# Optimization experiments

Measured on AMD Instinct MI355X. Metric: run time of the kernel, lower is better.

The kernel has to match this reference:

```python
import jax, jax.numpy as jnp
import numpy as np

N_NODES = 100000
N_HYPEREDGES = 20000
NNZ = 600000
D = 128


def setup_inputs() -> dict:
    key = jax.random.key(0)
    k = jax.random.split(key, 6)
    s = 1.0 / np.sqrt(D)
    x = jax.random.normal(k[0], (N_NODES, D), jnp.float32)
    node_idx = jax.random.randint(k[1], (NNZ,), 0, N_NODES, dtype=jnp.int64 if jax.config.jax_enable_x64 else jnp.int32)
    edge_idx = jax.random.randint(k[2], (NNZ,), 0, N_HYPEREDGES, dtype=jnp.int64 if jax.config.jax_enable_x64 else jnp.int32)
    conv_W = jax.random.uniform(k[3], (D, D), jnp.float32, -s, s)
    conv_b = jnp.zeros((D,), jnp.float32)
    res_W = jax.random.uniform(k[4], (D, D), jnp.float32, -s, s)
    res_b = jax.random.uniform(k[5], (D,), jnp.float32, -s, s)
    return {"x": x, "node_idx": node_idx, "edge_idx": edge_idx,
            "conv_W": conv_W, "conv_b": conv_b, "res_W": res_W, "res_b": res_b}


def hypergraph_conv(x, node_idx, edge_idx, W, b):
    # PyG HypergraphConv (no attention, unit hyperedge weights):
    #   out = D^{-1} H B^{-1} H^T (x W) + b
    y = x @ W                                                      # [N, D]
    ones = jnp.ones(node_idx.shape, dtype=y.dtype)
    deg_n = jax.ops.segment_sum(ones, node_idx, num_segments=N_NODES)        # node degree
    deg_e = jax.ops.segment_sum(ones, edge_idx, num_segments=N_HYPEREDGES)   # hyperedge size
    inv_n = jnp.where(deg_n > 0, 1.0 / deg_n, 0.0)
    inv_e = jnp.where(deg_e > 0, 1.0 / deg_e, 0.0)
    # node -> hyperedge aggregation, normalized by B^{-1}
    e_feat = jax.ops.segment_sum(y[node_idx], edge_idx, num_segments=N_HYPEREDGES)
    e_feat = e_feat * inv_e[:, None]                               # [E, D]
    # hyperedge -> node aggregation, normalized by D^{-1}
    out = jax.ops.segment_sum(e_feat[edge_idx], node_idx, num_segments=N_NODES)
    out = out * inv_n[:, None]                                     # [N, D]
    return out + b


def reference(x, node_idx, edge_idx, conv_W, conv_b, res_W, res_b):
    h = hypergraph_conv(x, node_idx, edge_idx, conv_W, conv_b)     # layer_num = 1
    return (x @ res_W + res_b) + h                                 # residual Linear + conv out
```

## Files before the change

kernel.cpp:

```cpp
#include <hip/hip_runtime.h>

#define N_NODES 100000
#define N_EDGES 20000
#define NNZ_C   600000
#define D 128

typedef short bf16x8 __attribute__((ext_vector_type(8)));
typedef float f32x4  __attribute__((ext_vector_type(4)));

__device__ __forceinline__ unsigned short f2bf(float f) {
    unsigned int u = __float_as_uint(f);
    u = (u + 0x7fffu + ((u >> 16) & 1u)) >> 16;
    return (unsigned short)u;
}
__device__ __forceinline__ float bf2f(unsigned short h) {
    return __uint_as_float((unsigned int)h << 16);
}
__device__ __forceinline__ unsigned int pk_trunc(float lo, float hi) {
    return __builtin_amdgcn_perm(__float_as_uint(hi), __float_as_uint(lo),
                                 0x07060302);
}

#define CHA 4096
#define NBLK_A 147
#define EW 313
#define NBE 64
#define NW 782
#define NBN 128
#define BCAP_E 12288
#define BCAP_N 6144

__global__ __launch_bounds__(256) void bin_pass(
    const int* __restrict__ nidx, const int* __restrict__ eidx,
    const float* __restrict__ cW, const float* __restrict__ rW,
    unsigned short* __restrict__ wtc, unsigned short* __restrict__ wtr,
    int* __restrict__ bucket_e, int* __restrict__ bucket_n,
    int* __restrict__ gcur_e, int* __restrict__ gcur_n) {
    const int bid = blockIdx.x;
    if (bid >= NBLK_A) {
        const int t0 = (bid - NBLK_A) * 4096;
        for (int i = threadIdx.x; i < 4096; i += 256) {
            const int t = t0 + i;
            const int m = t >> 14, idx = t & 16383;
            const int f = idx & 127, k = idx >> 7;
            const float* src = m ? rW : cW;
            unsigned short* dst = m ? wtr : wtc;
            dst[f * D + k] = f2bf(src[k * D + f]);
        }
        return;
    }
    const int jbeg = bid * CHA;
    const int jend = (jbeg + CHA < NNZ_C) ? jbeg + CHA : NNZ_C;
    __shared__ int cnt_e[NBE], base_e[NBE];
    __shared__ int cnt_n[NBN], base_n[NBN];
    for (int i = threadIdx.x; i < NBE; i += 256) cnt_e[i] = 0;
    for (int i = threadIdx.x; i < NBN; i += 256) cnt_n[i] = 0;
    __syncthreads();
    for (int j = jbeg + threadIdx.x; j < jend; j += 256) {
        atomicAdd(&cnt_e[eidx[j] / EW], 1);
        atomicAdd(&cnt_n[nidx[j] / NW], 1);
    }
    __syncthreads();
    for (int i = threadIdx.x; i < NBE; i += 256) {
        const int c = cnt_e[i];
        base_e[i] = c ? atomicAdd(&gcur_e[i], c) : 0;
        cnt_e[i] = 0;
    }
    for (int i = threadIdx.x; i < NBN; i += 256) {
        const int c = cnt_n[i];
        base_n[i] = c ? atomicAdd(&gcur_n[i], c) : 0;
        cnt_n[i] = 0;
    }
    __syncthreads();
    for (int j = jbeg + threadIdx.x; j < jend; j += 256) {
        const int e = eidx[j], n = nidx[j];
        {
            const int b = e / EW;
            const int p = ((e - b * EW) << 17) | n;
            const int pos = base_e[b] + atomicAdd(&cnt_e[b], 1);
            if (pos < BCAP_E) bucket_e[b * BCAP_E + pos] = p;
        }
        {
            const int b = n / NW;
            const int p = ((n - b * NW) << 15) | e;
            const int pos = base_n[b] + atomicAdd(&cnt_n[b], 1);
            if (pos < BCAP_N) bucket_n[b * BCAP_N + pos] = p;
        }
    }
}

__global__ __launch_bounds__(256) void scatter_pass(
    const int* __restrict__ bucket_e, const int* __restrict__ bucket_n,
    const int* __restrict__ gcur_e, const int* __restrict__ gcur_n,
    int* __restrict__ eptr, int* __restrict__ nptr,
    int* __restrict__ enodes, int* __restrict__ nedges) {
    __shared__ int vals[BCAP_E];
    __shared__ int cur[1024];
    __shared__ int red[256];
    const int tid = threadIdx.x;
    const int b = blockIdx.x;
    const int side = b >= NBE;
    const int cb = side ? b - NBE : b;
    const int* gc = side ? gcur_n : gcur_e;
    const int cap = side ? BCAP_N : BCAP_E;
    const int shift = side ? 15 : 17;
    const int mask = (1 << shift) - 1;
    const int width = side ? NW : EW;
    const int L = side ? N_NODES : N_EDGES;
    const int lo = cb * width;
    const int nbins = (lo + width < L) ? width : L - lo;
    const int* src = side ? (bucket_n + cb * BCAP_N) : (bucket_e + cb * BCAP_E);
    int* ptr = side ? nptr : eptr;
    int* dstG = side ? nedges : enodes;

    int part = 0;
    for (int i = tid; i < cb; i += 256) part += gc[i];
    red[tid] = part;
    __syncthreads();
    for (int off = 128; off > 0; off >>= 1) {
        if (tid < off) red[tid] += red[tid + off];
        __syncthreads();
    }
    const int bbase = red[0];
    int W = gc[cb];
    if (W > cap) W = cap;
    __syncthreads();

    for (int i = tid; i < 1024; i += 256) cur[i] = 0;
    __syncthreads();
    for (int i = tid; i < W; i += 256) atomicAdd(&cur[src[i] >> shift], 1);
    __syncthreads();

    int local[4];
    int s = 0;
#pragma unroll
    for (int k = 0; k < 4; ++k) {
        local[k] = s;
        s += cur[tid * 4 + k];
    }
    __syncthreads();
    red[tid] = s;
    __syncthreads();
    for (int off = 1; off < 256; off <<= 1) {
        const int t = (tid >= off) ? red[tid - off] : 0;
        __syncthreads();
        red[tid] += t;
        __syncthreads();
    }
    const int tb = red[tid] - s + bbase;
#pragma unroll
    for (int k = 0; k < 4; ++k) {
        const int idx = tid * 4 + k;
        if (idx < nbins) {
            const int v = tb + local[k];
            cur[idx] = v;
            ptr[lo + idx] = v;
        }
    }
    if (tid == 0 && cb == (side ? NBN - 1 : NBE - 1)) ptr[L] = NNZ_C;
    __syncthreads();

    for (int i = tid; i < W; i += 256) {
        const int p = src[i];
        const int slot = atomicAdd(&cur[p >> shift], 1) - bbase;
        if (slot < BCAP_E) vals[slot] = p & mask;
        else dstG[bbase + slot] = p & mask;
    }
    __syncthreads();
    const int lim = (W < BCAP_E) ? W : BCAP_E;
    for (int i = tid; i < lim; i += 256) dstG[bbase + i] = vals[i];
}

#define GT 64
#define XPAD 136
#define NTILES ((N_NODES + GT - 1) / GT)

__device__ __forceinline__ void stage_tile(unsigned short* __restrict__ buf,
                                           const float* __restrict__ x,
                                           int tile, int r0, int qp) {
    int n = tile * GT + r0;
    if (n >= N_NODES) n = N_NODES - 1;
    const float* xr = x + (size_t)n * D + qp * 16;
    unsigned short* dst = buf + r0 * XPAD + qp * 16;
#pragma unroll
    for (int u = 0; u < 2; ++u) {
        const float4 a = *(const float4*)(xr + u * 8);
        const float4 c = *(const float4*)(xr + u * 8 + 4);
        uint4 v;
        v.x = pk_trunc(a.x, a.y);
        v.y = pk_trunc(a.z, a.w);
        v.z = pk_trunc(c.x, c.y);
        v.w = pk_trunc(c.z, c.w);
        *(uint4*)(dst + u * 8) = v;
    }
}

__device__ __forceinline__ void compute_tile(
    const unsigned short* __restrict__ buf, const bf16x8 (&A)[2][4],
    int tile, int mat, int fh, int quad, int l16,
    unsigned short* __restrict__ yb, unsigned short* __restrict__ resb) {
    f32x4 acc[4][2] = {};
#pragma unroll
    for (int g = 0; g < 4; ++g)
#pragma unroll
        for (int kc = 0; kc < 4; ++kc) {
            const bf16x8 B = *(const bf16x8*)(buf + (g * 16 + l16) * XPAD +
                                              kc * 32 + quad * 8);
            acc[g][0] = __builtin_amdgcn_mfma_f32_16x16x32_bf16(A[0][kc], B, acc[g][0], 0, 0, 0);
            acc[g][1] = __builtin_amdgcn_mfma_f32_16x16x32_bf16(A[1][kc], B, acc[g][1], 0, 0, 0);
        }
    const int nbase = tile * GT;
    unsigned short* dst = mat ? resb : yb;
#pragma unroll
    for (int g = 0; g < 4; ++g) {
        const int n = nbase + g * 16 + l16;
        if (n >= N_NODES) continue;
#pragma unroll
        for (int ft = 0; ft < 2; ++ft) {
            const int f0 = fh + ft * 16 + quad * 4;
            uint2 v;
            v.x = pk_trunc(acc[g][ft][0], acc[g][ft][1]);
            v.y = pk_trunc(acc[g][ft][2], acc[g][ft][3]);
            *(uint2*)(dst + (size_t)n * D + f0) = v;
        }
    }
}

__global__ __launch_bounds__(512) void mfma_gemm(
    const float* __restrict__ x, const unsigned short* __restrict__ wtc,
    const unsigned short* __restrict__ wtr,
    unsigned short* __restrict__ yb, unsigned short* __restrict__ resb) {
    __shared__ unsigned short xs[2][GT * XPAD];

    const int w    = threadIdx.x >> 6;
    const int lane = threadIdx.x & 63;
    const int quad = lane >> 4;
    const int l16  = lane & 15;
    const int mat  = w & 1;
    const int fh   = (w >> 1) * 32;

    const unsigned short* wsrc = mat ? wtr : wtc;
    bf16x8 A[2][4];
#pragma unroll
    for (int ft = 0; ft < 2; ++ft)
#pragma unroll
        for (int kc = 0; kc < 4; ++kc)
            A[ft][kc] = *(const bf16x8*)(wsrc + (fh + ft * 16 + l16) * D +
                                         kc * 32 + quad * 8);

    const int r0 = threadIdx.x >> 3;
    const int qp = threadIdx.x & 7;
    const int t0 = blockIdx.x * 2;

    stage_tile(xs[0], x, t0, r0, qp);
    __syncthreads();
    stage_tile(xs[1], x, t0 + 1, r0, qp);
    compute_tile(xs[0], A, t0, mat, fh, quad, l16, yb, resb);
    __syncthreads();
    compute_tile(xs[1], A, t0 + 1, mat, fh, quad, l16, yb, resb);
}

__global__ __launch_bounds__(256) void edge_aggregate(
    const unsigned short* __restrict__ yb, const int* __restrict__ eptr,
    const int* __restrict__ enodes, unsigned short* __restrict__ efb) {
    const int e = blockIdx.x * 16 + (threadIdx.x >> 4);
    const int l = threadIdx.x & 15;
    const int beg = eptr[e], end = eptr[e + 1];
    float acc[8] = {};
    int j = beg;
    for (; j + 4 <= end; j += 4) {
        const int n0 = enodes[j], n1 = enodes[j + 1];
        const int n2 = enodes[j + 2], n3 = enodes[j + 3];
        const bf16x8 p0 = *(const bf16x8*)(yb + (size_t)n0 * D + l * 8);
        const bf16x8 p1 = *(const bf16x8*)(yb + (size_t)n1 * D + l * 8);
        const bf16x8 p2 = *(const bf16x8*)(yb + (size_t)n2 * D + l * 8);
        const bf16x8 p3 = *(const bf16x8*)(yb + (size_t)n3 * D + l * 8);
#pragma unroll
        for (int i = 0; i < 8; ++i)
            acc[i] += (bf2f((unsigned short)p0[i]) + bf2f((unsigned short)p1[i]))
                    + (bf2f((unsigned short)p2[i]) + bf2f((unsigned short)p3[i]));
    }
    for (; j < end; ++j) {
        const bf16x8 p = *(const bf16x8*)(yb + (size_t)enodes[j] * D + l * 8);
#pragma unroll
        for (int i = 0; i < 8; ++i) acc[i] += bf2f((unsigned short)p[i]);
    }
    const int deg = end - beg;
    const float inv = deg ? 1.f / (float)deg : 0.f;
    bf16x8 o;
#pragma unroll
    for (int i = 0; i < 8; ++i) o[i] = (short)f2bf(acc[i] * inv);
    *(bf16x8*)(efb + (size_t)e * D + l * 8) = o;
}

__global__ __launch_bounds__(256) void node_aggregate(
    const unsigned short* __restrict__ efb, const int* __restrict__ nptr,
    const int* __restrict__ nedges, const unsigned short* __restrict__ resb,
    const float* __restrict__ rb, const float* __restrict__ cb,
    float* __restrict__ out) {
    const int n = blockIdx.x * 16 + (threadIdx.x >> 4);
    const int l = threadIdx.x & 15;
    const int beg = nptr[n], end = nptr[n + 1];
    float acc[8] = {};
    int j = beg;
    for (; j + 2 <= end; j += 2) {
        const int e0 = nedges[j], e1 = nedges[j + 1];
        const bf16x8 p0 = *(const bf16x8*)(efb + (size_t)e0 * D + l * 8);
        const bf16x8 p1 = *(const bf16x8*)(efb + (size_t)e1 * D + l * 8);
#pragma unroll
        for (int i = 0; i < 8; ++i)
            acc[i] += bf2f((unsigned short)p0[i]) + bf2f((unsigned short)p1[i]);
    }
    if (j < end) {
        const bf16x8 p = *(const bf16x8*)(efb + (size_t)nedges[j] * D + l * 8);
#pragma unroll
        for (int i = 0; i < 8; ++i) acc[i] += bf2f((unsigned short)p[i]);
    }
    const int deg = end - beg;
    const float inv = deg ? 1.f / (float)deg : 0.f;
    const bf16x8 r = *(const bf16x8*)(resb + (size_t)n * D + l * 8);
    const float4 rb0 = *(const float4*)(rb + l * 8);
    const float4 rb1 = *(const float4*)(rb + l * 8 + 4);
    const float4 cb0 = *(const float4*)(cb + l * 8);
    const float4 cb1 = *(const float4*)(cb + l * 8 + 4);
    float4 o0, o1;
    o0.x = bf2f((unsigned short)r[0]) + acc[0] * inv + rb0.x + cb0.x;
    o0.y = bf2f((unsigned short)r[1]) + acc[1] * inv + rb0.y + cb0.y;
    o0.z = bf2f((unsigned short)r[2]) + acc[2] * inv + rb0.z + cb0.z;
    o0.w = bf2f((unsigned short)r[3]) + acc[3] * inv + rb0.w + cb0.w;
    o1.x = bf2f((unsigned short)r[4]) + acc[4] * inv + rb1.x + cb1.x;
    o1.y = bf2f((unsigned short)r[5]) + acc[5] * inv + rb1.y + cb1.y;
    o1.z = bf2f((unsigned short)r[6]) + acc[6] * inv + rb1.z + cb1.z;
    o1.w = bf2f((unsigned short)r[7]) + acc[7] * inv + rb1.w + cb1.w;
    const size_t o = (size_t)n * D + l * 8;
    *(float4*)(out + o) = o0;
    *(float4*)(out + o + 4) = o1;
}

extern "C" void kernel_launch(void* const* d_in, const int* in_sizes, int n_in,
                              void* d_out, int out_size, void* d_ws,
                              size_t ws_size, hipStream_t stream) {
    const float* x  = (const float*)d_in[0];
    const int* nidx = (const int*)d_in[1];
    const int* eidx = (const int*)d_in[2];
    const float* cW = (const float*)d_in[3];
    const float* cb = (const float*)d_in[4];
    const float* rW = (const float*)d_in[5];
    const float* rb = (const float*)d_in[6];
    float* out = (float*)d_out;

    char* ws = (char*)d_ws;
    size_t off = 0;
    auto alloc = [&](size_t bytes) {
        size_t o = off;
        off += (bytes + 255) & ~(size_t)255;
        return o;
    };
    unsigned short* yb   = (unsigned short*)(ws + alloc((size_t)N_NODES * D * 2));
    unsigned short* resb = (unsigned short*)(ws + alloc((size_t)N_NODES * D * 2));
    unsigned short* efb  = (unsigned short*)(ws + alloc((size_t)N_EDGES * D * 2));
    unsigned short* wtc  = (unsigned short*)(ws + alloc((size_t)D * D * 2));
    unsigned short* wtr  = (unsigned short*)(ws + alloc((size_t)D * D * 2));
    int* enodes   = (int*)(ws + alloc((size_t)NNZ_C * 4));
    int* nedges   = (int*)(ws + alloc((size_t)NNZ_C * 4));
    int* eptr     = (int*)(ws + alloc((size_t)(N_EDGES + 1) * 4));
    int* nptr     = (int*)(ws + alloc((size_t)(N_NODES + 1) * 4));
    int* bucket_e = (int*)(ws + alloc((size_t)NBE * BCAP_E * 4));
    int* bucket_n = (int*)(ws + alloc((size_t)NBN * BCAP_N * 4));
    int* gcur     = (int*)(ws + alloc((size_t)(NBE + NBN) * 4));
    int* gcur_e = gcur;
    int* gcur_n = gcur + NBE;

    hipMemsetAsync(gcur, 0, (size_t)(NBE + NBN) * 4, stream);

    bin_pass<<<NBLK_A + 8, 256, 0, stream>>>(nidx, eidx, cW, rW, wtc, wtr,
                                             bucket_e, bucket_n, gcur_e, gcur_n);

    mfma_gemm<<<(NTILES + 1) / 2, 512, 0, stream>>>(x, wtc, wtr, yb, resb);

    scatter_pass<<<NBE + NBN, 256, 0, stream>>>(bucket_e, bucket_n,
                                                gcur_e, gcur_n,
                                                eptr, nptr, enodes, nedges);

    edge_aggregate<<<N_EDGES / 16, 256, 0, stream>>>(yb, eptr, enodes, efb);
    node_aggregate<<<N_NODES / 16, 256, 0, stream>>>(efb, nptr, nedges, resb,
                                                     rb, cb, out);
}
```

Measured before the change: 220.7 us.

## Fuse CSR scatter into aggregation kernels using fine 32-wide buckets

Drops the separate scatter_pass that built global CSR arrays. Instead, bin_pass buckets incidences into many small 32-id buckets, and each aggregation block sorts its own bucket in shared memory before gathering. This removes one kernel launch and the global CSR write and re-read, but shrinks aggregation blocks to 32 rows with 2 rows per 16-lane group. It also enlarges bin_pass's shared histograms to 625+3125 counters, which makes the per-block setup and atomic reservation loops heavier. Fixed per-bucket capacities (1536/512) risk dropping entries if a bucket overflows, although with random indices the expected loads are about 960 and 192.

```diff
diff --git a/kernel.cpp b/kernel.cpp
--- a/kernel.cpp
+++ b/kernel.cpp
@@ -21,14 +21,14 @@
                                  0x07060302);
 }
 
-#define CHA 4096
-#define NBLK_A 147
-#define EW 313
-#define NBE 64
-#define NW 782
-#define NBN 128
-#define BCAP_E 12288
-#define BCAP_N 6144
+#define CHA 8192
+#define NBLK_A 74
+#define EBW 32
+#define NBE 625
+#define ECAP 1536
+#define NBW 32
+#define NBN 3125
+#define NCAP 512
 
 __global__ __launch_bounds__(256) void bin_pass(
     const int* __restrict__ nidx, const int* __restrict__ eidx,
@@ -57,8 +57,8 @@
     for (int i = threadIdx.x; i < NBN; i += 256) cnt_n[i] = 0;
     __syncthreads();
     for (int j = jbeg + threadIdx.x; j < jend; j += 256) {
-        atomicAdd(&cnt_e[eidx[j] / EW], 1);
-        atomicAdd(&cnt_n[nidx[j] / NW], 1);
+        atomicAdd(&cnt_e[eidx[j] >> 5], 1);
+        atomicAdd(&cnt_n[nidx[j] >> 5], 1);
     }
     __syncthreads();
     for (int i = threadIdx.x; i < NBE; i += 256) {
@@ -75,100 +75,16 @@
     for (int j = jbeg + threadIdx.x; j < jend; j += 256) {
         const int e = eidx[j], n = nidx[j];
         {
-            const int b = e / EW;
-            const int p = ((e - b * EW) << 17) | n;
+            const int b = e >> 5;
             const int pos = base_e[b] + atomicAdd(&cnt_e[b], 1);
-            if (pos < BCAP_E) bucket_e[b * BCAP_E + pos] = p;
+            if (pos < ECAP) bucket_e[b * ECAP + pos] = ((e & 31) << 17) | n;
         }
         {
-            const int b = n / NW;
-            const int p = ((n - b * NW) << 15) | e;
+            const int b = n >> 5;
             const int pos = base_n[b] + atomicAdd(&cnt_n[b], 1);
-            if (pos < BCAP_N) bucket_n[b * BCAP_N + pos] = p;
-        }
-    }
-}
-
-__global__ __launch_bounds__(256) void scatter_pass(
-    const int* __restrict__ bucket_e, const int* __restrict__ bucket_n,
-    const int* __restrict__ gcur_e, const int* __restrict__ gcur_n,
-    int* __restrict__ eptr, int* __restrict__ nptr,
-    int* __restrict__ enodes, int* __restrict__ nedges) {
-    __shared__ int vals[BCAP_E];
-    __shared__ int cur[1024];
-    __shared__ int red[256];
-    const int tid = threadIdx.x;
-    const int b = blockIdx.x;
-    const int side = b >= NBE;
-    const int cb = side ? b - NBE : b;
-    const int* gc = side ? gcur_n : gcur_e;
-    const int cap = side ? BCAP_N : BCAP_E;
-    const int shift = side ? 15 : 17;
-    const int mask = (1 << shift) - 1;
-    const int width = side ? NW : EW;
-    const int L = side ? N_NODES : N_EDGES;
-    const int lo = cb * width;
-    const int nbins = (lo + width < L) ? width : L - lo;
-    const int* src = side ? (bucket_n + cb * BCAP_N) : (bucket_e + cb * BCAP_E);
-    int* ptr = side ? nptr : eptr;
-    int* dstG = side ? nedges : enodes;
-
-    int part = 0;
-    for (int i = tid; i < cb; i += 256) part += gc[i];
-    red[tid] = part;
-    __syncthreads();
-    for (int off = 128; off > 0; off >>= 1) {
-        if (tid < off) red[tid] += red[tid + off];
-        __syncthreads();
-    }
-    const int bbase = red[0];
-    int W = gc[cb];
-    if (W > cap) W = cap;
-    __syncthreads();
-
-    for (int i = tid; i < 1024; i += 256) cur[i] = 0;
-    __syncthreads();
-    for (int i = tid; i < W; i += 256) atomicAdd(&cur[src[i] >> shift], 1);
-    __syncthreads();
-
-    int local[4];
-    int s = 0;
-#pragma unroll
-    for (int k = 0; k < 4; ++k) {
-        local[k] = s;
-        s += cur[tid * 4 + k];
-    }
-    __syncthreads();
-    red[tid] = s;
-    __syncthreads();
-    for (int off = 1; off < 256; off <<= 1) {
-        const int t = (tid >= off) ? red[tid - off] : 0;
-        __syncthreads();
-        red[tid] += t;
-        __syncthreads();
-    }
-    const int tb = red[tid] - s + bbase;
-#pragma unroll
-    for (int k = 0; k < 4; ++k) {
-        const int idx = tid * 4 + k;
-        if (idx < nbins) {
-            const int v = tb + local[k];
-            cur[idx] = v;
-            ptr[lo + idx] = v;
-        }
-    }
-    if (tid == 0 && cb == (side ? NBN - 1 : NBE - 1)) ptr[L] = NNZ_C;
-    __syncthreads();
-
-    for (int i = tid; i < W; i += 256) {
-        const int p = src[i];
-        const int slot = atomicAdd(&cur[p >> shift], 1) - bbase;
-        if (slot < BCAP_E) vals[slot] = p & mask;
-        else dstG[bbase + slot] = p & mask;
-    }
-    __syncthreads();
-    const int lim = (W < BCAP_E) ? W : BCAP_E;
-    for (int i = tid; i < lim; i += 256) dstG[bbase + i] = vals[i];
+            if (pos < NCAP) bucket_n[b * NCAP + pos] = ((n & 31) << 15) | e;
+        }
+    }
 }
 
 #define GT 64
@@ -261,80 +177,163 @@
 }
 
 __global__ __launch_bounds__(256) void edge_aggregate(
-    const unsigned short* __restrict__ yb, const int* __restrict__ eptr,
-    const int* __restrict__ enodes, unsigned short* __restrict__ efb) {
-    const int e = blockIdx.x * 16 + (threadIdx.x >> 4);
-    const int l = threadIdx.x & 15;
-    const int beg = eptr[e], end = eptr[e + 1];
-    float acc[8] = {};
-    int j = beg;
-    for (; j + 4 <= end; j += 4) {
-        const int n0 = enodes[j], n1 = enodes[j + 1];
-        const int n2 = enodes[j + 2], n3 = enodes[j + 3];
-        const bf16x8 p0 = *(const bf16x8*)(yb + (size_t)n0 * D + l * 8);
-        const bf16x8 p1 = *(const bf16x8*)(yb + (size_t)n1 * D + l * 8);
-        const bf16x8 p2 = *(const bf16x8*)(yb + (size_t)n2 * D + l * 8);
-        const bf16x8 p3 = *(const bf16x8*)(yb + (size_t)n3 * D + l * 8);
-#pragma unroll
-        for (int i = 0; i < 8; ++i)
-            acc[i] += (bf2f((unsigned short)p0[i]) + bf2f((unsigned short)p1[i]))
-                    + (bf2f((unsigned short)p2[i]) + bf2f((unsigned short)p3[i]));
-    }
-    for (; j < end; ++j) {
-        const bf16x8 p = *(const bf16x8*)(yb + (size_t)enodes[j] * D + l * 8);
-#pragma unroll
-        for (int i = 0; i < 8; ++i) acc[i] += bf2f((unsigned short)p[i]);
-    }
-    const int deg = end - beg;
-    const float inv = deg ? 1.f / (float)deg : 0.f;
-    bf16x8 o;
-#pragma unroll
-    for (int i = 0; i < 8; ++i) o[i] = (short)f2bf(acc[i] * inv);
-    *(bf16x8*)(efb + (size_t)e * D + l * 8) = o;
+    const int* __restrict__ bucket_e, const int* __restrict__ gcur_e,
+    const unsigned short* __restrict__ yb, unsigned short* __restrict__ efb) {
+    __shared__ int raw[ECAP];
+    __shared__ int srt[ECAP];
+    __shared__ int cnt[EBW + 1];
+    __shared__ int cur[EBW];
+    const int tid = threadIdx.x;
+    const int b = blockIdx.x;
+    int W = gcur_e[b];
+    if (W > ECAP) W = ECAP;
+    if (tid < EBW + 1) cnt[tid] = 0;
+    __syncthreads();
+    const int* src = bucket_e + b * ECAP;
+    for (int i = tid; i < W; i += 256) {
+        const int p = src[i];
+        raw[i] = p;
+        atomicAdd(&cnt[p >> 17], 1);
+    }
+    __syncthreads();
+    if (tid < EBW) {
+        const int c = cnt[tid];
+        int v = c;
+#pragma unroll
+        for (int off = 1; off < EBW; off <<= 1) {
+            const int t = __shfl_up(v, off);
+            if (tid >= off) v += t;
+        }
+        cnt[tid] = v - c;
+        cur[tid] = v - c;
+        if (tid == EBW - 1) cnt[EBW] = v;
+    }
+    __syncthreads();
+    for (int i = tid; i < W; i += 256) {
+        const int p = raw[i];
+        const int pos = atomicAdd(&cur[p >> 17], 1);
+        srt[pos] = p & 0x1FFFF;
+    }
+    __syncthreads();
+
+    const int g = tid >> 4;
+    const int l = tid & 15;
+#pragma unroll
+    for (int u = 0; u < 2; ++u) {
+        const int el = g * 2 + u;
+        const int beg = cnt[el], end = cnt[el + 1];
+        float acc[8] = {};
+        int j = beg;
+        for (; j + 4 <= end; j += 4) {
+            const int n0 = srt[j], n1 = srt[j + 1];
+            const int n2 = srt[j + 2], n3 = srt[j + 3];
+            const bf16x8 p0 = *(const bf16x8*)(yb + (size_t)n0 * D + l * 8);
+            const bf16x8 p1 = *(const bf16x8*)(yb + (size_t)n1 * D + l * 8);
+            const bf16x8 p2 = *(const bf16x8*)(yb + (size_t)n2 * D + l * 8);
+            const bf16x8 p3 = *(const bf16x8*)(yb + (size_t)n3 * D + l * 8);
+#pragma unroll
+            for (int i = 0; i < 8; ++i)
+                acc[i] += (bf2f((unsigned short)p0[i]) + bf2f((unsigned short)p1[i]))
+                        + (bf2f((unsigned short)p2[i]) + bf2f((unsigned short)p3[i]));
+        }
+        for (; j < end; ++j) {
+            const bf16x8 p = *(const bf16x8*)(yb + (size_t)srt[j] * D + l * 8);
+#pragma unroll
+            for (int i = 0; i < 8; ++i) acc[i] += bf2f((unsigned short)p[i]);
+        }
+        const int deg = end - beg;
+        const float inv = deg ? 1.f / (float)deg : 0.f;
+        bf16x8 o;
+#pragma unroll
+        for (int i = 0; i < 8; ++i) o[i] = (short)f2bf(acc[i] * inv);
+        *(bf16x8*)(efb + (size_t)(b * EBW + el) * D + l * 8) = o;
+    }
 }
 
 __global__ __launch_bounds__(256) void node_aggregate(
-    const unsigned short* __restrict__ efb, const int* __restrict__ nptr,
-    const int* __restrict__ nedges, const unsigned short* __restrict__ resb,
+    const int* __restrict__ bucket_n, const int* __restrict__ gcur_n,
+    const unsigned short* __restrict__ efb, const unsigned short* __restrict__ resb,
     const float* __restrict__ rb, const float* __restrict__ cb,
     float* __restrict__ out) {
-    const int n = blockIdx.x * 16 + (threadIdx.x >> 4);
-    const int l = threadIdx.x & 15;
-    const int beg = nptr[n], end = nptr[n + 1];
-    float acc[8] = {};
-    int j = beg;
-    for (; j + 2 <= end; j += 2) {
-        const int e0 = nedges[j], e1 = nedges[j + 1];
-        const bf16x8 p0 = *(const bf16x8*)(efb + (size_t)e0 * D + l * 8);
-        const bf16x8 p1 = *(const bf16x8*)(efb + (size_t)e1 * D + l * 8);
-#pragma unroll
-        for (int i = 0; i < 8; ++i)
-            acc[i] += bf2f((unsigned short)p0[i]) + bf2f((unsigned short)p1[i]);
-    }
-    if (j < end) {
-        const bf16x8 p = *(const bf16x8*)(efb + (size_t)nedges[j] * D + l * 8);
-#pragma unroll
-        for (int i = 0; i < 8; ++i) acc[i] += bf2f((unsigned short)p[i]);
-    }
-    const int deg = end - beg;
-    const float inv = deg ? 1.f / (float)deg : 0.f;
-    const bf16x8 r = *(const bf16x8*)(resb + (size_t)n * D + l * 8);
-    const float4 rb0 = *(const float4*)(rb + l * 8);
-    const float4 rb1 = *(const float4*)(rb + l * 8 + 4);
-    const float4 cb0 = *(const float4*)(cb + l * 8);
-    const float4 cb1 = *(const float4*)(cb + l * 8 + 4);
-    float4 o0, o1;
-    o0.x = bf2f((unsigned short)r[0]) + acc[0] * inv + rb0.x + cb0.x;
-    o0.y = bf2f((unsigned short)r[1]) + acc[1] * inv + rb0.y + cb0.y;
-    o0.z = bf2f((unsigned short)r[2]) + acc[2] * inv + rb0.z + cb0.z;
-    o0.w = bf2f((unsigned short)r[3]) + acc[3] * inv + rb0.w + cb0.w;
-    o1.x = bf2f((unsigned short)r[4]) + acc[4] * inv + rb1.x + cb1.x;
-    o1.y = bf2f((unsigned short)r[5]) + acc[5] * inv + rb1.y + cb1.y;
-    o1.z = bf2f((unsigned short)r[6]) + acc[6] * inv + rb1.z + cb1.z;
-    o1.w = bf2f((unsigned short)r[7]) + acc[7] * inv + rb1.w + cb1.w;
-    const size_t o = (size_t)n * D + l * 8;
-    *(float4*)(out + o) = o0;
-    *(float4*)(out + o + 4) = o1;
+    __shared__ int raw[NCAP];
+    __shared__ int srt[NCAP];
+    __shared__ int cnt[NBW + 1];
+    __shared__ int cur[NBW];
+    const int tid = threadIdx.x;
+    const int b = blockIdx.x;
+    int W = gcur_n[b];
+    if (W > NCAP) W = NCAP;
+    if (tid < NBW + 1) cnt[tid] = 0;
+    __syncthreads();
+    const int* src = bucket_n + b * NCAP;
+    for (int i = tid; i < W; i += 256) {
+        const int p = src[i];
+        raw[i] = p;
+        atomicAdd(&cnt[p >> 15], 1);
+    }
+    __syncthreads();
+    if (tid < NBW) {
+        const int c = cnt[tid];
+        int v = c;
+#pragma unroll
+        for (int off = 1; off < NBW; off <<= 1) {
+            const int t = __shfl_up(v, off);
+            if (tid >= off) v += t;
+        }
+        cnt[tid] = v - c;
+        cur[tid] = v - c;
+        if (tid == NBW - 1) cnt[NBW] = v;
+    }
+    __syncthreads();
+    for (int i = tid; i < W; i += 256) {
+        const int p = raw[i];
+        const int pos = atomicAdd(&cur[p >> 15], 1);
+        srt[pos] = p & 0x7FFF;
+    }
+    __syncthreads();
+
+    const int g = tid >> 4;
+    const int l = tid & 15;
+#pragma unroll
+    for (int u = 0; u < 2; ++u) {
+        const int nl = g * 2 + u;
+        const int n = b * NBW + nl;
+        const int beg = cnt[nl], end = cnt[nl + 1];
+        float acc[8] = {};
+        int j = beg;
+        for (; j + 2 <= end; j += 2) {
+            const int e0 = srt[j], e1 = srt[j + 1];
+            const bf16x8 p0 = *(const bf16x8*)(efb + (size_t)e0 * D + l * 8);
+            const bf16x8 p1 = *(const bf16x8*)(efb + (size_t)e1 * D + l * 8);
+#pragma unroll
+            for (int i = 0; i < 8; ++i)
+                acc[i] += bf2f((unsigned short)p0[i]) + bf2f((unsigned short)p1[i]);
+        }
+        if (j < end) {
+            const bf16x8 p = *(const bf16x8*)(efb + (size_t)srt[j] * D + l * 8);
+#pragma unroll
+            for (int i = 0; i < 8; ++i) acc[i] += bf2f((unsigned short)p[i]);
+        }
+        const int deg = end - beg;
+        const float inv = deg ? 1.f / (float)deg : 0.f;
+        const bf16x8 r = *(const bf16x8*)(resb + (size_t)n * D + l * 8);
+        const float4 rb0 = *(const float4*)(rb + l * 8);
+        const float4 rb1 = *(const float4*)(rb + l * 8 + 4);
+        const float4 cb0 = *(const float4*)(cb + l * 8);
+        const float4 cb1 = *(const float4*)(cb + l * 8 + 4);
+        float4 o0, o1;
+        o0.x = bf2f((unsigned short)r[0]) + acc[0] * inv + rb0.x + cb0.x;
+        o0.y = bf2f((unsigned short)r[1]) + acc[1] * inv + rb0.y + cb0.y;
+        o0.z = bf2f((unsigned short)r[2]) + acc[2] * inv + rb0.z + cb0.z;
+        o0.w = bf2f((unsigned short)r[3]) + acc[3] * inv + rb0.w + cb0.w;
+        o1.x = bf2f((unsigned short)r[4]) + acc[4] * inv + rb1.x + cb1.x;
+        o1.y = bf2f((unsigned short)r[5]) + acc[5] * inv + rb1.y + cb1.y;
+        o1.z = bf2f((unsigned short)r[6]) + acc[6] * inv + rb1.z + cb1.z;
+        o1.w = bf2f((unsigned short)r[7]) + acc[7] * inv + rb1.w + cb1.w;
+        const size_t o = (size_t)n * D + l * 8;
+        *(float4*)(out + o) = o0;
+        *(float4*)(out + o + 4) = o1;
+    }
 }
 
 extern "C" void kernel_launch(void* const* d_in, const int* in_sizes, int n_in,
@@ -361,12 +360,8 @@
     unsigned short* efb  = (unsigned short*)(ws + alloc((size_t)N_EDGES * D * 2));
     unsigned short* wtc  = (unsigned short*)(ws + alloc((size_t)D * D * 2));
     unsigned short* wtr  = (unsigned short*)(ws + alloc((size_t)D * D * 2));
-    int* enodes   = (int*)(ws + alloc((size_t)NNZ_C * 4));
-    int* nedges   = (int*)(ws + alloc((size_t)NNZ_C * 4));
-    int* eptr     = (int*)(ws + alloc((size_t)(N_EDGES + 1) * 4));
-    int* nptr     = (int*)(ws + alloc((size_t)(N_NODES + 1) * 4));
-    int* bucket_e = (int*)(ws + alloc((size_t)NBE * BCAP_E * 4));
-    int* bucket_n = (int*)(ws + alloc((size_t)NBN * BCAP_N * 4));
+    int* bucket_e = (int*)(ws + alloc((size_t)NBE * ECAP * 4));
+    int* bucket_n = (int*)(ws + alloc((size_t)NBN * NCAP * 4));
     int* gcur     = (int*)(ws + alloc((size_t)(NBE + NBN) * 4));
     int* gcur_e = gcur;
     int* gcur_n = gcur + NBE;
@@ -378,11 +373,7 @@
 
     mfma_gemm<<<(NTILES + 1) / 2, 512, 0, stream>>>(x, wtc, wtr, yb, resb);
 
-    scatter_pass<<<NBE + NBN, 256, 0, stream>>>(bucket_e, bucket_n,
-                                                gcur_e, gcur_n,
-                                                eptr, nptr, enodes, nedges);
-
-    edge_aggregate<<<N_EDGES / 16, 256, 0, stream>>>(yb, eptr, enodes, efb);
-    node_aggregate<<<N_NODES / 16, 256, 0, stream>>>(efb, nptr, nedges, resb,
-                                                     rb, cb, out);
-}
+    edge_aggregate<<<NBE, 256, 0, stream>>>(bucket_e, gcur_e, yb, efb);
+    node_aggregate<<<NBN, 256, 0, stream>>>(bucket_n, gcur_n, efb, resb,
+                                            rb, cb, out);
+}
```

Measured after the change: 220.1 us. No clear change (-0.3%).

## Rework CSR build with power-of-two megabuckets and shared-memory local sorting

Applied to the files above, without the earlier changes.

Replaces the two-pass binning (count, then scatter with global atomics per element) with a block-local counting sort in shared memory, so each block writes contiguous runs into more, smaller power-of-two megabuckets (shift instead of divide). The global bucket cursors are padded to separate cache lines to reduce atomic contention. The repartition kernel now stages each bucket in LDS, sorts it there and writes the output coalesced. It launches more blocks for both passes and adds extra LDS use and barriers per block.

```diff
diff --git a/kernel.cpp b/kernel.cpp
--- a/kernel.cpp
+++ b/kernel.cpp
@@ -21,25 +21,33 @@
                                  0x07060302);
 }
 
-#define CHA 4096
-#define NBLK_A 147
-#define EW 313
-#define NBE 64
-#define NW 782
-#define NBN 128
-#define BCAP_E 12288
-#define BCAP_N 6144
-
-__global__ __launch_bounds__(256) void bin_pass(
+#define CH 2048
+#define NBLK_A 293
+#define EMW 128
+#define NME 157
+#define EMCAP 4352
+#define NMW 512
+#define NMN 196
+#define NMCAP 3584
+#define PADI 32
+#define GCUR_INTS ((NME + NMN) * PADI)
+
+__global__ __launch_bounds__(256) void bin_coarse(
     const int* __restrict__ nidx, const int* __restrict__ eidx,
     const float* __restrict__ cW, const float* __restrict__ rW,
     unsigned short* __restrict__ wtc, unsigned short* __restrict__ wtr,
     int* __restrict__ bucket_e, int* __restrict__ bucket_n,
     int* __restrict__ gcur_e, int* __restrict__ gcur_n) {
+    __shared__ int rawE[CH], rawN[CH];
+    __shared__ int srt[CH];
+    __shared__ unsigned char sbin[CH];
+    __shared__ int red[256];
+    __shared__ int cnt[NMN], lbase[NMN], gbase[NMN], cur[NMN];
     const int bid = blockIdx.x;
+    const int tid = threadIdx.x;
     if (bid >= NBLK_A) {
         const int t0 = (bid - NBLK_A) * 4096;
-        for (int i = threadIdx.x; i < 4096; i += 256) {
+        for (int i = tid; i < 4096; i += 256) {
             const int t = t0 + i;
             const int m = t >> 14, idx = t & 16383;
             const int f = idx & 127, k = idx >> 7;
@@ -49,72 +57,93 @@
         }
         return;
     }
-    const int jbeg = bid * CHA;
-    const int jend = (jbeg + CHA < NNZ_C) ? jbeg + CHA : NNZ_C;
-    __shared__ int cnt_e[NBE], base_e[NBE];
-    __shared__ int cnt_n[NBN], base_n[NBN];
-    for (int i = threadIdx.x; i < NBE; i += 256) cnt_e[i] = 0;
-    for (int i = threadIdx.x; i < NBN; i += 256) cnt_n[i] = 0;
-    __syncthreads();
-    for (int j = jbeg + threadIdx.x; j < jend; j += 256) {
-        atomicAdd(&cnt_e[eidx[j] / EW], 1);
-        atomicAdd(&cnt_n[nidx[j] / NW], 1);
-    }
-    __syncthreads();
-    for (int i = threadIdx.x; i < NBE; i += 256) {
-        const int c = cnt_e[i];
-        base_e[i] = c ? atomicAdd(&gcur_e[i], c) : 0;
-        cnt_e[i] = 0;
-    }
-    for (int i = threadIdx.x; i < NBN; i += 256) {
-        const int c = cnt_n[i];
-        base_n[i] = c ? atomicAdd(&gcur_n[i], c) : 0;
-        cnt_n[i] = 0;
-    }
-    __syncthreads();
-    for (int j = jbeg + threadIdx.x; j < jend; j += 256) {
-        const int e = eidx[j], n = nidx[j];
-        {
-            const int b = e / EW;
-            const int p = ((e - b * EW) << 17) | n;
-            const int pos = base_e[b] + atomicAdd(&cnt_e[b], 1);
-            if (pos < BCAP_E) bucket_e[b * BCAP_E + pos] = p;
-        }
-        {
-            const int b = n / NW;
-            const int p = ((n - b * NW) << 15) | e;
-            const int pos = base_n[b] + atomicAdd(&cnt_n[b], 1);
-            if (pos < BCAP_N) bucket_n[b * BCAP_N + pos] = p;
-        }
-    }
-}
-
-__global__ __launch_bounds__(256) void scatter_pass(
+    const int j0 = bid * CH;
+    const int jn = (j0 + CH < NNZ_C) ? CH : NNZ_C - j0;
+    for (int i = tid; i < jn; i += 256) {
+        rawE[i] = eidx[j0 + i];
+        rawN[i] = nidx[j0 + i];
+    }
+    __syncthreads();
+
+#pragma unroll
+    for (int s = 0; s < 2; ++s) {
+        const int nb = s ? NMN : NME;
+        int* gc = s ? gcur_n : gcur_e;
+        int* dst = s ? bucket_n : bucket_e;
+        const int cap = s ? NMCAP : EMCAP;
+        for (int i = tid; i < nb; i += 256) cnt[i] = 0;
+        __syncthreads();
+        for (int i = tid; i < jn; i += 256) {
+            const int b = s ? (rawN[i] >> 9) : (rawE[i] >> 7);
+            atomicAdd(&cnt[b], 1);
+        }
+        __syncthreads();
+        const int v = (tid < nb) ? cnt[tid] : 0;
+        red[tid] = v;
+        __syncthreads();
+        for (int off = 1; off < 256; off <<= 1) {
+            const int t = (tid >= off) ? red[tid - off] : 0;
+            __syncthreads();
+            red[tid] += t;
+            __syncthreads();
+        }
+        const int excl = red[tid] - v;
+        if (tid < nb) {
+            lbase[tid] = excl;
+            cur[tid] = excl;
+            gbase[tid] = v ? atomicAdd(&gc[tid * PADI], v) : 0;
+        }
+        __syncthreads();
+        for (int i = tid; i < jn; i += 256) {
+            const int e = rawE[i], n = rawN[i];
+            const int b = s ? (n >> 9) : (e >> 7);
+            const int pk = s ? (((n & 511) << 15) | e) : (((e & 127) << 17) | n);
+            const int pos = atomicAdd(&cur[b], 1);
+            srt[pos] = pk;
+            sbin[pos] = (unsigned char)b;
+        }
+        __syncthreads();
+        for (int i = tid; i < jn; i += 256) {
+            const int b = sbin[i];
+            const int off2 = gbase[b] + (i - lbase[b]);
+            if (off2 < cap) dst[b * cap + off2] = srt[i];
+        }
+        __syncthreads();
+    }
+}
+
+__global__ __launch_bounds__(256) void repartition(
     const int* __restrict__ bucket_e, const int* __restrict__ bucket_n,
     const int* __restrict__ gcur_e, const int* __restrict__ gcur_n,
     int* __restrict__ eptr, int* __restrict__ nptr,
     int* __restrict__ enodes, int* __restrict__ nedges) {
-    __shared__ int vals[BCAP_E];
-    __shared__ int cur[1024];
+    __shared__ int raw[EMCAP];
+    __shared__ int srt[EMCAP];
+    __shared__ int cnt[NMW + 1];
+    __shared__ int cur[NMW];
     __shared__ int red[256];
     const int tid = threadIdx.x;
     const int b = blockIdx.x;
-    const int side = b >= NBE;
-    const int cb = side ? b - NBE : b;
-    const int* gc = side ? gcur_n : gcur_e;
-    const int cap = side ? BCAP_N : BCAP_E;
+    const int side = b >= NME;
+    const int cb = side ? b - NME : b;
+    const int nbf = side ? NMW : EMW;
+    const int L = side ? N_NODES : N_EDGES;
+    const int lo = cb * nbf;
+    const int nbins = (lo + nbf < L) ? nbf : L - lo;
+    const int cap = side ? NMCAP : EMCAP;
     const int shift = side ? 15 : 17;
     const int mask = (1 << shift) - 1;
-    const int width = side ? NW : EW;
-    const int L = side ? N_NODES : N_EDGES;
-    const int lo = cb * width;
-    const int nbins = (lo + width < L) ? width : L - lo;
-    const int* src = side ? (bucket_n + cb * BCAP_N) : (bucket_e + cb * BCAP_E);
+    const int nmega = side ? NMN : NME;
+    const int* gc = side ? gcur_n : gcur_e;
+    const int* src = side ? bucket_n + cb * NMCAP : bucket_e + cb * EMCAP;
     int* ptr = side ? nptr : eptr;
     int* dstG = side ? nedges : enodes;
 
     int part = 0;
-    for (int i = tid; i < cb; i += 256) part += gc[i];
+    for (int i = tid; i < cb; i += 256) {
+        int c = gc[i * PADI];
+        part += (c < cap) ? c : cap;
+    }
     red[tid] = part;
     __syncthreads();
     for (int off = 128; off > 0; off >>= 1) {
@@ -122,24 +151,21 @@
         __syncthreads();
     }
     const int bbase = red[0];
-    int W = gc[cb];
+    int W = gc[cb * PADI];
     if (W > cap) W = cap;
     __syncthreads();
 
-    for (int i = tid; i < 1024; i += 256) cur[i] = 0;
-    __syncthreads();
-    for (int i = tid; i < W; i += 256) atomicAdd(&cur[src[i] >> shift], 1);
-    __syncthreads();
-
-    int local[4];
-    int s = 0;
-#pragma unroll
-    for (int k = 0; k < 4; ++k) {
-        local[k] = s;
-        s += cur[tid * 4 + k];
-    }
-    __syncthreads();
-    red[tid] = s;
+    for (int i = tid; i < NMW + 1; i += 256) cnt[i] = 0;
+    __syncthreads();
+    for (int i = tid; i < W; i += 256) {
+        const int p = src[i];
+        raw[i] = p;
+        atomicAdd(&cnt[p >> shift], 1);
+    }
+    __syncthreads();
+    const int a0 = cnt[tid * 2], a1 = cnt[tid * 2 + 1];
+    const int sum = a0 + a1;
+    red[tid] = sum;
     __syncthreads();
     for (int off = 1; off < 256; off <<= 1) {
         const int t = (tid >= off) ? red[tid - off] : 0;
@@ -147,28 +173,22 @@
         red[tid] += t;
         __syncthreads();
     }
-    const int tb = red[tid] - s + bbase;
-#pragma unroll
-    for (int k = 0; k < 4; ++k) {
-        const int idx = tid * 4 + k;
-        if (idx < nbins) {
-            const int v = tb + local[k];
-            cur[idx] = v;
-            ptr[lo + idx] = v;
-        }
-    }
-    if (tid == 0 && cb == (side ? NBN - 1 : NBE - 1)) ptr[L] = NNZ_C;
-    __syncthreads();
-
+    const int excl = red[tid] - sum;
+    cnt[tid * 2] = excl;
+    cnt[tid * 2 + 1] = excl + a0;
+    cur[tid * 2] = excl;
+    cur[tid * 2 + 1] = excl + a0;
+    __syncthreads();
+    for (int i = tid; i < nbins; i += 256) ptr[lo + i] = bbase + cnt[i];
+    if (cb == nmega - 1 && tid == 0) ptr[L] = bbase + W;
+    __syncthreads();
     for (int i = tid; i < W; i += 256) {
-        const int p = src[i];
-        const int slot = atomicAdd(&cur[p >> shift], 1) - bbase;
-        if (slot < BCAP_E) vals[slot] = p & mask;
-        else dstG[bbase + slot] = p & mask;
-    }
-    __syncthreads();
-    const int lim = (W < BCAP_E) ? W : BCAP_E;
-    for (int i = tid; i < lim; i += 256) dstG[bbase + i] = vals[i];
+        const int p = raw[i];
+        const int pos = atomicAdd(&cur[p >> shift], 1);
+        srt[pos] = p & mask;
+    }
+    __syncthreads();
+    for (int i = tid; i < W; i += 256) dstG[bbase + i] = srt[i];
 }
 
 #define GT 64
@@ -361,26 +381,26 @@
     unsigned short* efb  = (unsigned short*)(ws + alloc((size_t)N_EDGES * D * 2));
     unsigned short* wtc  = (unsigned short*)(ws + alloc((size_t)D * D * 2));
     unsigned short* wtr  = (unsigned short*)(ws + alloc((size_t)D * D * 2));
+    int* bucket_e = (int*)(ws + alloc((size_t)NME * EMCAP * 4));
+    int* bucket_n = (int*)(ws + alloc((size_t)NMN * NMCAP * 4));
     int* enodes   = (int*)(ws + alloc((size_t)NNZ_C * 4));
     int* nedges   = (int*)(ws + alloc((size_t)NNZ_C * 4));
     int* eptr     = (int*)(ws + alloc((size_t)(N_EDGES + 1) * 4));
     int* nptr     = (int*)(ws + alloc((size_t)(N_NODES + 1) * 4));
-    int* bucket_e = (int*)(ws + alloc((size_t)NBE * BCAP_E * 4));
-    int* bucket_n = (int*)(ws + alloc((size_t)NBN * BCAP_N * 4));
-    int* gcur     = (int*)(ws + alloc((size_t)(NBE + NBN) * 4));
+    int* gcur     = (int*)(ws + alloc((size_t)GCUR_INTS * 4));
     int* gcur_e = gcur;
-    int* gcur_n = gcur + NBE;
-
-    hipMemsetAsync(gcur, 0, (size_t)(NBE + NBN) * 4, stream);
-
-    bin_pass<<<NBLK_A + 8, 256, 0, stream>>>(nidx, eidx, cW, rW, wtc, wtr,
-                                             bucket_e, bucket_n, gcur_e, gcur_n);
+    int* gcur_n = gcur + NME * PADI;
+
+    hipMemsetAsync(gcur, 0, (size_t)GCUR_INTS * 4, stream);
+
+    bin_coarse<<<NBLK_A + 8, 256, 0, stream>>>(nidx, eidx, cW, rW, wtc, wtr,
+                                               bucket_e, bucket_n, gcur_e, gcur_n);
 
     mfma_gemm<<<(NTILES + 1) / 2, 512, 0, stream>>>(x, wtc, wtr, yb, resb);
 
-    scatter_pass<<<NBE + NBN, 256, 0, stream>>>(bucket_e, bucket_n,
-                                                gcur_e, gcur_n,
-                                                eptr, nptr, enodes, nedges);
+    repartition<<<NME + NMN, 256, 0, stream>>>(bucket_e, bucket_n,
+                                               gcur_e, gcur_n,
+                                               eptr, nptr, enodes, nedges);
 
     edge_aggregate<<<N_EDGES / 16, 256, 0, stream>>>(yb, eptr, enodes, efb);
     node_aggregate<<<N_NODES / 16, 256, 0, stream>>>(efb, nptr, nedges, resb,
```

New measurement: 203.4 us. 7.8% less time.
